# Performance work log

Hardware: AMD Instinct MI355X
Metric: run time of the kernel (lower is better)

Reference implementation:

```python
import jax, jax.numpy as jnp
import numpy as np

B, H, S, D = 4, 8, 8192, 64


def setup_inputs() -> dict:
    key = jax.random.key(0)
    kq, kk, kv_, kqm, kkm = jax.random.split(key, 5)
    q = jax.random.normal(kq, (B, H, S, D), dtype=jnp.float32)
    k = jax.random.normal(kk, (B, H, S, D), dtype=jnp.float32)
    v = jax.random.normal(kv_, (B, H, S, D), dtype=jnp.float32)
    q_mask = jax.random.randint(kqm, (B, S), 0, 2).astype(jnp.bool_)
    kv_mask = jax.random.randint(kkm, (B, S), 0, 2).astype(jnp.bool_)
    return {"q": q, "k": k, "v": v, "q_mask": q_mask, "kv_mask": kv_mask}


def reference(q, k, v, q_mask, kv_mask):
    # Linear (kernelized) attention branch: feature map phi(x) = elu(x) + 1
    qe = jax.nn.elu(q) + 1.0
    ke = jax.nn.elu(k) + 1.0
    qm = q_mask.astype(q.dtype)[:, None, :, None]   # [B,1,S,1]
    km = kv_mask.astype(q.dtype)[:, None, :, None]
    qe = qe * qm
    ke = ke * km
    ve = v * km
    s = v.shape[2]
    # kv: [B,H,D,D] contraction over kv sequence
    kv = jnp.einsum('bhsd,bhsc->bhdc', ke, ve / s)
    # normalizer per query position: [B,H,L]
    div = 1.0 / (jnp.einsum('bhld,bhsd->bhl', qe, ke) + 1e-6)
    out = s * jnp.einsum('bhld,bhdc,bhl->bhlc', qe, kv, div)
    return out
```

## Files before the change

### kernel.cpp

```cpp
#include <hip/hip_runtime.h>
#include <hip/hip_bf16.h>


#define S_LEN 8192
#define NBH 32
#define KVSTRIDE 4160

typedef __attribute__((ext_vector_type(8))) short short8;
typedef __attribute__((ext_vector_type(4))) float f32x4;

__device__ __forceinline__ float elu1(float x) {
  return x > 0.0f ? (x + 1.0f) : __expf(x);
}
__device__ __forceinline__ unsigned short f2bf(float x) {
  __hip_bfloat16 h = __float2bfloat16(x);
  union { __hip_bfloat16 b; unsigned short u; } cv; cv.b = h; return cv.u;
}
__device__ __forceinline__ float bf2f(unsigned short u) {
  return __uint_as_float(((unsigned)u) << 16);
}
__device__ __forceinline__ void split2(float x, unsigned short& hi, unsigned short& lo) {
  hi = f2bf(x);
  lo = f2bf(x - bf2f(hi));
}
__device__ __forceinline__ short8 ones8() {
  short8 o;
#pragma unroll
  for (int i = 0; i < 8; ++i) o[i] = (short)0x3F80;
  return o;
}

#define MFMA(a,b,c) __builtin_amdgcn_mfma_f32_16x16x32_bf16((a),(b),(c),0,0,0)

__global__ __launch_bounds__(256) void k1_partial(
    const float* __restrict__ kin, const float* __restrict__ vin,
    const int* __restrict__ kv_mask, float* __restrict__ partials, int seg_rows) {
  __shared__ unsigned short keT_h[64 * 72];
  __shared__ unsigned short keT_l[64 * 72];
  __shared__ unsigned short veT_h[64 * 72];
  __shared__ unsigned short veT_l[64 * 72];
  const int tid = threadIdx.x;
  const int seg = blockIdx.x, bh = blockIdx.y, b = bh >> 3;
  const int dp = tid & 31;
  const int so = tid >> 5;
  const int lane = tid & 63, w = tid >> 6;
  const int mrow = lane & 15, qd4 = lane >> 4;
  const short8 one = ones8();

  f32x4 acc[4]; f32x4 accs;
#pragma unroll
  for (int t = 0; t < 4; ++t) acc[t] = (f32x4){0.f, 0.f, 0.f, 0.f};
  accs = (f32x4){0.f, 0.f, 0.f, 0.f};

  const int rbase = seg * seg_rows;
  for (int t0 = 0; t0 < seg_rows; t0 += 64) {
    const int r0 = rbase + t0;
    const float* kp = kin + ((size_t)bh * S_LEN + r0 + so * 8) * 64 + dp * 2;
    const float* vp = vin + ((size_t)bh * S_LEN + r0 + so * 8) * 64 + dp * 2;
    union { unsigned short u[8]; uint4 v; } kh0, kh1, kl0, kl1, vh0, vh1, vl0, vl1;
#pragma unroll
    for (int r = 0; r < 8; ++r) {
      float m = kv_mask[b * S_LEN + r0 + so * 8 + r] ? 1.0f : 0.0f;
      float2 kw = *(const float2*)(kp + (size_t)r * 64);
      float2 vw = *(const float2*)(vp + (size_t)r * 64);
      float ka = elu1(kw.x) * m;
      float kb = elu1(kw.y) * m;
      float mv = m * (1.0f / 8192.0f);
      float va = vw.x * mv, vb = vw.y * mv;
      split2(ka, kh0.u[r], kl0.u[r]);
      split2(kb, kh1.u[r], kl1.u[r]);
      split2(va, vh0.u[r], vl0.u[r]);
      split2(vb, vh1.u[r], vl1.u[r]);
    }
    const int d0 = dp * 2;
    *(uint4*)&keT_h[(d0    ) * 72 + so * 8] = kh0.v;
    *(uint4*)&keT_h[(d0 + 1) * 72 + so * 8] = kh1.v;
    *(uint4*)&keT_l[(d0    ) * 72 + so * 8] = kl0.v;
    *(uint4*)&keT_l[(d0 + 1) * 72 + so * 8] = kl1.v;
    *(uint4*)&veT_h[(d0    ) * 72 + so * 8] = vh0.v;
    *(uint4*)&veT_h[(d0 + 1) * 72 + so * 8] = vh1.v;
    *(uint4*)&veT_l[(d0    ) * 72 + so * 8] = vl0.v;
    *(uint4*)&veT_l[(d0 + 1) * 72 + so * 8] = vl1.v;
    __syncthreads();
#pragma unroll
    for (int k0 = 0; k0 < 64; k0 += 32) {
      short8 a_h = *(const short8*)&keT_h[(w * 16 + mrow) * 72 + k0 + qd4 * 8];
      short8 a_l = *(const short8*)&keT_l[(w * 16 + mrow) * 72 + k0 + qd4 * 8];
      accs = MFMA(a_h, one, accs);
      accs = MFMA(a_l, one, accs);
#pragma unroll
      for (int t = 0; t < 4; ++t) {
        short8 b_h = *(const short8*)&veT_h[(t * 16 + mrow) * 72 + k0 + qd4 * 8];
        short8 b_l = *(const short8*)&veT_l[(t * 16 + mrow) * 72 + k0 + qd4 * 8];
        acc[t] = MFMA(a_h, b_h, acc[t]);
        acc[t] = MFMA(a_h, b_l, acc[t]);
        acc[t] = MFMA(a_l, b_h, acc[t]);
      }
    }
    __syncthreads();
  }
  float* p = partials + ((size_t)bh * gridDim.x + seg) * KVSTRIDE;
#pragma unroll
  for (int t = 0; t < 4; ++t)
#pragma unroll
    for (int r = 0; r < 4; ++r)
      p[(w * 16 + qd4 * 4 + r) * 64 + t * 16 + mrow] = acc[t][r];
  if (mrow == 0) {
#pragma unroll
    for (int r = 0; r < 4; ++r) p[4096 + w * 16 + qd4 * 4 + r] = accs[r];
  }
}

__global__ __launch_bounds__(256) void k2_reduce(
    const float* __restrict__ partials,
    unsigned short* __restrict__ kvTh, unsigned short* __restrict__ kvTl,
    unsigned short* __restrict__ ksh, unsigned short* __restrict__ ksl, int nchunk) {
  const int idx = blockIdx.x * 256 + threadIdx.x;
  if (idx >= NBH * KVSTRIDE) return;
  const int bh = idx / KVSTRIDE;
  const int e = idx - bh * KVSTRIDE;
  const float* p = partials + (size_t)bh * nchunk * KVSTRIDE + e;
  float s0 = 0.f, s1 = 0.f, s2 = 0.f, s3 = 0.f;
  int c = 0;
  for (; c + 4 <= nchunk; c += 4) {
    s0 += p[(size_t)(c + 0) * KVSTRIDE];
    s1 += p[(size_t)(c + 1) * KVSTRIDE];
    s2 += p[(size_t)(c + 2) * KVSTRIDE];
    s3 += p[(size_t)(c + 3) * KVSTRIDE];
  }
  for (; c < nchunk; ++c) s0 += p[(size_t)c * KVSTRIDE];
  float s = (s0 + s1) + (s2 + s3);
  unsigned short hi, lo;
  split2(s, hi, lo);
  if (e < 4096) {
    int d = e >> 6, cc = e & 63;
    kvTh[(size_t)bh * 4096 + cc * 64 + d] = hi;
    kvTl[(size_t)bh * 4096 + cc * 64 + d] = lo;
  } else {
    int d = e - 4096;
    ksh[bh * 64 + d] = hi;
    ksl[bh * 64 + d] = lo;
  }
}

__global__ __launch_bounds__(256) void k3_out(
    const float* __restrict__ qin, const int* __restrict__ q_mask,
    const unsigned short* __restrict__ kvTh_g, const unsigned short* __restrict__ kvTl_g,
    const unsigned short* __restrict__ ksh_g, const unsigned short* __restrict__ ksl_g,
    float* __restrict__ out) {
  __shared__ unsigned short qe_h[64 * 72];
  __shared__ unsigned short qe_l[64 * 72];
  __shared__ unsigned short kv_h[64 * 72];
  __shared__ unsigned short kv_l[64 * 72];
  __shared__ __align__(16) unsigned short ks_h[64];
  __shared__ __align__(16) unsigned short ks_l[64];
  const int tid = threadIdx.x;
  const int rb = blockIdx.x, bh = blockIdx.y, b = bh >> 3;
  const int r0 = rb * 64;
#pragma unroll
  for (int i = 0; i < 4; ++i) {
    int qd = i * 256 + tid;
    int l = qd >> 4, dq = qd & 15;
    float m = q_mask[b * S_LEN + r0 + l] ? 1.0f : 0.0f;
    float4 qw = *(const float4*)(qin + ((size_t)bh * S_LEN + r0 + l) * 64 + dq * 4);
    union { unsigned short u[4]; uint2 v; } h, lo;
    float e0 = elu1(qw.x) * m, e1 = elu1(qw.y) * m, e2 = elu1(qw.z) * m, e3 = elu1(qw.w) * m;
    split2(e0, h.u[0], lo.u[0]);
    split2(e1, h.u[1], lo.u[1]);
    split2(e2, h.u[2], lo.u[2]);
    split2(e3, h.u[3], lo.u[3]);
    *(uint2*)&qe_h[l * 72 + dq * 4] = h.v;
    *(uint2*)&qe_l[l * 72 + dq * 4] = lo.v;
  }
  for (int e = tid; e < 2048; e += 256) {
    int c = (e * 2) >> 6, d = (e * 2) & 63;
    *(unsigned*)&kv_h[c * 72 + d] = *(const unsigned*)(kvTh_g + (size_t)bh * 4096 + e * 2);
    *(unsigned*)&kv_l[c * 72 + d] = *(const unsigned*)(kvTl_g + (size_t)bh * 4096 + e * 2);
  }
  if (tid < 64) {
    ks_h[tid] = ksh_g[bh * 64 + tid];
    ks_l[tid] = ksl_g[bh * 64 + tid];
  }
  __syncthreads();
  const int lane = tid & 63, w = tid >> 6;
  const int mrow = lane & 15, qd4 = lane >> 4;
  f32x4 acc[4]; f32x4 accd;
#pragma unroll
  for (int t = 0; t < 4; ++t) acc[t] = (f32x4){0.f, 0.f, 0.f, 0.f};
  accd = (f32x4){0.f, 0.f, 0.f, 0.f};
#pragma unroll
  for (int k0 = 0; k0 < 64; k0 += 32) {
    short8 a_h = *(const short8*)&qe_h[(w * 16 + mrow) * 72 + k0 + qd4 * 8];
    short8 a_l = *(const short8*)&qe_l[(w * 16 + mrow) * 72 + k0 + qd4 * 8];
    short8 s_h = *(const short8*)&ks_h[k0 + qd4 * 8];
    short8 s_l = *(const short8*)&ks_l[k0 + qd4 * 8];
    accd = MFMA(a_h, s_h, accd);
    accd = MFMA(a_h, s_l, accd);
    accd = MFMA(a_l, s_h, accd);
#pragma unroll
    for (int t = 0; t < 4; ++t) {
      short8 b_h = *(const short8*)&kv_h[(t * 16 + mrow) * 72 + k0 + qd4 * 8];
      short8 b_l = *(const short8*)&kv_l[(t * 16 + mrow) * 72 + k0 + qd4 * 8];
      acc[t] = MFMA(a_h, b_h, acc[t]);
      acc[t] = MFMA(a_h, b_l, acc[t]);
      acc[t] = MFMA(a_l, b_h, acc[t]);
    }
  }
#pragma unroll
  for (int r = 0; r < 4; ++r) {
    float inv = 8192.0f / (accd[r] + 1e-6f);
    int row = r0 + w * 16 + qd4 * 4 + r;
#pragma unroll
    for (int t = 0; t < 4; ++t)
      out[((size_t)bh * S_LEN + row) * 64 + t * 16 + mrow] = acc[t][r] * inv;
  }
}

extern "C" void kernel_launch(void* const* d_in, const int* in_sizes, int n_in,
                              void* d_out, int out_size, void* d_ws, size_t ws_size,
                              hipStream_t stream) {
  const float* q = (const float*)d_in[0];
  const float* k = (const float*)d_in[1];
  const float* v = (const float*)d_in[2];
  const int* qm = (const int*)d_in[3];
  const int* km = (const int*)d_in[4];
  float* out = (float*)d_out;

  int nchunk = 32;
  while (nchunk > 1) {
    size_t need = (size_t)NBH * nchunk * KVSTRIDE * 4
                + (size_t)NBH * 4096 * 2 * 2 + (size_t)NBH * 64 * 2 * 2;
    if (need <= ws_size) break;
    nchunk >>= 1;
  }
  float* partials = (float*)d_ws;
  unsigned short* kvTh = (unsigned short*)(partials + (size_t)NBH * nchunk * KVSTRIDE);
  unsigned short* kvTl = kvTh + (size_t)NBH * 4096;
  unsigned short* ksh  = kvTl + (size_t)NBH * 4096;
  unsigned short* ksl  = ksh + NBH * 64;
  int seg_rows = S_LEN / nchunk;

  k1_partial<<<dim3(nchunk, NBH), 256, 0, stream>>>(k, v, km, partials, seg_rows);
  int n_elem = NBH * KVSTRIDE;
  k2_reduce<<<dim3((n_elem + 255) / 256), 256, 0, stream>>>(partials, kvTh, kvTl, ksh, ksl, nchunk);
  k3_out<<<dim3(S_LEN / 64, NBH), 256, 0, stream>>>(q, qm, kvTh, kvTl, ksh, ksl, out);
}
```

Before: 238.5 us.

## Drop LDS staging: build MFMA fragments directly from global loads in both kernels

k1 now gives each wave its own sequence segment and builds the bf16 hi/lo MFMA operands straight from global memory. This removes the shared-memory transpose and the block barriers. The K row-sum is done with scalar adds plus shuffles instead of MFMAs against a ones vector, and the chunk count doubles to 64 to keep parallelism up. k3 likewise loads Q and the KV tiles straight into registers with no LDS. The trade is strided, less coalesced global reads (column-wise per lane in k1), more register pressure from the 16 accumulators, and more partials for k2 to reduce.

```diff
diff --git a/kernel.cpp b/kernel.cpp
--- a/kernel.cpp
+++ b/kernel.cpp
@@ -13,8 +13,9 @@
   return x > 0.0f ? (x + 1.0f) : __expf(x);
 }
 __device__ __forceinline__ unsigned short f2bf(float x) {
-  __hip_bfloat16 h = __float2bfloat16(x);
-  union { __hip_bfloat16 b; unsigned short u; } cv; cv.b = h; return cv.u;
+  union { __hip_bfloat16 b; unsigned short u; } cv;
+  cv.b = __float2bfloat16(x);
+  return cv.u;
 }
 __device__ __forceinline__ float bf2f(unsigned short u) {
   return __uint_as_float(((unsigned)u) << 16);
@@ -23,91 +24,84 @@
   hi = f2bf(x);
   lo = f2bf(x - bf2f(hi));
 }
-__device__ __forceinline__ short8 ones8() {
-  short8 o;
-#pragma unroll
-  for (int i = 0; i < 8; ++i) o[i] = (short)0x3F80;
-  return o;
-}
 
 #define MFMA(a,b,c) __builtin_amdgcn_mfma_f32_16x16x32_bf16((a),(b),(c),0,0,0)
 
 __global__ __launch_bounds__(256) void k1_partial(
     const float* __restrict__ kin, const float* __restrict__ vin,
-    const int* __restrict__ kv_mask, float* __restrict__ partials, int seg_rows) {
-  __shared__ unsigned short keT_h[64 * 72];
-  __shared__ unsigned short keT_l[64 * 72];
-  __shared__ unsigned short veT_h[64 * 72];
-  __shared__ unsigned short veT_l[64 * 72];
+    const int* __restrict__ kv_mask, float* __restrict__ partials,
+    int nchunk, int seg_rows) {
   const int tid = threadIdx.x;
-  const int seg = blockIdx.x, bh = blockIdx.y, b = bh >> 3;
-  const int dp = tid & 31;
-  const int so = tid >> 5;
   const int lane = tid & 63, w = tid >> 6;
+  const int bh = blockIdx.y, b = bh >> 3;
+  const int seg = blockIdx.x * 4 + w;
   const int mrow = lane & 15, qd4 = lane >> 4;
-  const short8 one = ones8();
-
-  f32x4 acc[4]; f32x4 accs;
-#pragma unroll
-  for (int t = 0; t < 4; ++t) acc[t] = (f32x4){0.f, 0.f, 0.f, 0.f};
-  accs = (f32x4){0.f, 0.f, 0.f, 0.f};
-
-  const int rbase = seg * seg_rows;
-  for (int t0 = 0; t0 < seg_rows; t0 += 64) {
-    const int r0 = rbase + t0;
-    const float* kp = kin + ((size_t)bh * S_LEN + r0 + so * 8) * 64 + dp * 2;
-    const float* vp = vin + ((size_t)bh * S_LEN + r0 + so * 8) * 64 + dp * 2;
-    union { unsigned short u[8]; uint4 v; } kh0, kh1, kl0, kl1, vh0, vh1, vl0, vl1;
-#pragma unroll
-    for (int r = 0; r < 8; ++r) {
-      float m = kv_mask[b * S_LEN + r0 + so * 8 + r] ? 1.0f : 0.0f;
-      float2 kw = *(const float2*)(kp + (size_t)r * 64);
-      float2 vw = *(const float2*)(vp + (size_t)r * 64);
-      float ka = elu1(kw.x) * m;
-      float kb = elu1(kw.y) * m;
-      float mv = m * (1.0f / 8192.0f);
-      float va = vw.x * mv, vb = vw.y * mv;
-      split2(ka, kh0.u[r], kl0.u[r]);
-      split2(kb, kh1.u[r], kl1.u[r]);
-      split2(va, vh0.u[r], vl0.u[r]);
-      split2(vb, vh1.u[r], vl1.u[r]);
-    }
-    const int d0 = dp * 2;
-    *(uint4*)&keT_h[(d0    ) * 72 + so * 8] = kh0.v;
-    *(uint4*)&keT_h[(d0 + 1) * 72 + so * 8] = kh1.v;
-    *(uint4*)&keT_l[(d0    ) * 72 + so * 8] = kl0.v;
-    *(uint4*)&keT_l[(d0 + 1) * 72 + so * 8] = kl1.v;
-    *(uint4*)&veT_h[(d0    ) * 72 + so * 8] = vh0.v;
-    *(uint4*)&veT_h[(d0 + 1) * 72 + so * 8] = vh1.v;
-    *(uint4*)&veT_l[(d0    ) * 72 + so * 8] = vl0.v;
-    *(uint4*)&veT_l[(d0 + 1) * 72 + so * 8] = vl1.v;
-    __syncthreads();
-#pragma unroll
-    for (int k0 = 0; k0 < 64; k0 += 32) {
-      short8 a_h = *(const short8*)&keT_h[(w * 16 + mrow) * 72 + k0 + qd4 * 8];
-      short8 a_l = *(const short8*)&keT_l[(w * 16 + mrow) * 72 + k0 + qd4 * 8];
-      accs = MFMA(a_h, one, accs);
-      accs = MFMA(a_l, one, accs);
-#pragma unroll
-      for (int t = 0; t < 4; ++t) {
-        short8 b_h = *(const short8*)&veT_h[(t * 16 + mrow) * 72 + k0 + qd4 * 8];
-        short8 b_l = *(const short8*)&veT_l[(t * 16 + mrow) * 72 + k0 + qd4 * 8];
-        acc[t] = MFMA(a_h, b_h, acc[t]);
-        acc[t] = MFMA(a_h, b_l, acc[t]);
-        acc[t] = MFMA(a_l, b_h, acc[t]);
+
+  f32x4 acc[4][4];
+#pragma unroll
+  for (int i = 0; i < 4; ++i)
+#pragma unroll
+    for (int j = 0; j < 4; ++j) acc[i][j] = (f32x4){0.f, 0.f, 0.f, 0.f};
+  float ks[4] = {0.f, 0.f, 0.f, 0.f};
+
+  const float* kbase = kin + (size_t)bh * S_LEN * 64;
+  const float* vbase = vin + (size_t)bh * S_LEN * 64;
+  const int s_seg = seg * seg_rows;
+
+  for (int c0 = 0; c0 < seg_rows; c0 += 32) {
+    const int s0 = s_seg + c0 + qd4 * 8;
+    float mj[8];
+#pragma unroll
+    for (int j = 0; j < 8; ++j)
+      mj[j] = kv_mask[b * S_LEN + s0 + j] ? 1.0f : 0.0f;
+
+    short8 b_h[4], b_l[4];
+#pragma unroll
+    for (int td = 0; td < 4; ++td) {
+      const float* kp = kbase + (size_t)s0 * 64 + td * 16 + mrow;
+      union { unsigned short u[8]; short8 s8; } hh, ll;
+#pragma unroll
+      for (int j = 0; j < 8; ++j) {
+        float ke = elu1(kp[(size_t)j * 64]) * mj[j];
+        ks[td] += ke;
+        split2(ke, hh.u[j], ll.u[j]);
       }
-    }
-    __syncthreads();
-  }
-  float* p = partials + ((size_t)bh * gridDim.x + seg) * KVSTRIDE;
-#pragma unroll
-  for (int t = 0; t < 4; ++t)
-#pragma unroll
-    for (int r = 0; r < 4; ++r)
-      p[(w * 16 + qd4 * 4 + r) * 64 + t * 16 + mrow] = acc[t][r];
-  if (mrow == 0) {
-#pragma unroll
-    for (int r = 0; r < 4; ++r) p[4096 + w * 16 + qd4 * 4 + r] = accs[r];
+      b_h[td] = hh.s8; b_l[td] = ll.s8;
+    }
+#pragma unroll
+    for (int tc = 0; tc < 4; ++tc) {
+      const float* vp = vbase + (size_t)s0 * 64 + tc * 16 + mrow;
+      union { unsigned short u[8]; short8 s8; } hh, ll;
+#pragma unroll
+      for (int j = 0; j < 8; ++j) {
+        float ve = vp[(size_t)j * 64] * (mj[j] * (1.0f / 8192.0f));
+        split2(ve, hh.u[j], ll.u[j]);
+      }
+      short8 a_h = hh.s8, a_l = ll.s8;
+#pragma unroll
+      for (int td = 0; td < 4; ++td) {
+        acc[tc][td] = MFMA(a_h, b_h[td], acc[tc][td]);
+        acc[tc][td] = MFMA(a_h, b_l[td], acc[tc][td]);
+        acc[tc][td] = MFMA(a_l, b_h[td], acc[tc][td]);
+      }
+    }
+  }
+#pragma unroll
+  for (int td = 0; td < 4; ++td) {
+    ks[td] += __shfl_xor(ks[td], 32);
+    ks[td] += __shfl_xor(ks[td], 16);
+  }
+  float* p = partials + ((size_t)bh * nchunk + seg) * KVSTRIDE;
+#pragma unroll
+  for (int tc = 0; tc < 4; ++tc)
+#pragma unroll
+    for (int td = 0; td < 4; ++td)
+#pragma unroll
+      for (int r = 0; r < 4; ++r)
+        p[(tc * 16 + qd4 * 4 + r) * 64 + td * 16 + mrow] = acc[tc][td][r];
+  if (qd4 == 0) {
+#pragma unroll
+    for (int td = 0; td < 4; ++td) p[4096 + td * 16 + mrow] = ks[td];
   }
 }
 
@@ -133,86 +127,66 @@
   unsigned short hi, lo;
   split2(s, hi, lo);
   if (e < 4096) {
-    int d = e >> 6, cc = e & 63;
-    kvTh[(size_t)bh * 4096 + cc * 64 + d] = hi;
-    kvTl[(size_t)bh * 4096 + cc * 64 + d] = lo;
+    kvTh[(size_t)bh * 4096 + e] = hi;
+    kvTl[(size_t)bh * 4096 + e] = lo;
   } else {
-    int d = e - 4096;
-    ksh[bh * 64 + d] = hi;
-    ksl[bh * 64 + d] = lo;
+    ksh[bh * 64 + (e - 4096)] = hi;
+    ksl[bh * 64 + (e - 4096)] = lo;
   }
 }
 
 __global__ __launch_bounds__(256) void k3_out(
     const float* __restrict__ qin, const int* __restrict__ q_mask,
-    const unsigned short* __restrict__ kvTh_g, const unsigned short* __restrict__ kvTl_g,
-    const unsigned short* __restrict__ ksh_g, const unsigned short* __restrict__ ksl_g,
+    const unsigned short* __restrict__ kvTh, const unsigned short* __restrict__ kvTl,
+    const unsigned short* __restrict__ ksh, const unsigned short* __restrict__ ksl,
     float* __restrict__ out) {
-  __shared__ unsigned short qe_h[64 * 72];
-  __shared__ unsigned short qe_l[64 * 72];
-  __shared__ unsigned short kv_h[64 * 72];
-  __shared__ unsigned short kv_l[64 * 72];
-  __shared__ __align__(16) unsigned short ks_h[64];
-  __shared__ __align__(16) unsigned short ks_l[64];
-  const int tid = threadIdx.x;
+  const int tid = threadIdx.x, lane = tid & 63, w = tid >> 6;
   const int rb = blockIdx.x, bh = blockIdx.y, b = bh >> 3;
-  const int r0 = rb * 64;
-#pragma unroll
-  for (int i = 0; i < 4; ++i) {
-    int qd = i * 256 + tid;
-    int l = qd >> 4, dq = qd & 15;
-    float m = q_mask[b * S_LEN + r0 + l] ? 1.0f : 0.0f;
-    float4 qw = *(const float4*)(qin + ((size_t)bh * S_LEN + r0 + l) * 64 + dq * 4);
-    union { unsigned short u[4]; uint2 v; } h, lo;
-    float e0 = elu1(qw.x) * m, e1 = elu1(qw.y) * m, e2 = elu1(qw.z) * m, e3 = elu1(qw.w) * m;
-    split2(e0, h.u[0], lo.u[0]);
-    split2(e1, h.u[1], lo.u[1]);
-    split2(e2, h.u[2], lo.u[2]);
-    split2(e3, h.u[3], lo.u[3]);
-    *(uint2*)&qe_h[l * 72 + dq * 4] = h.v;
-    *(uint2*)&qe_l[l * 72 + dq * 4] = lo.v;
-  }
-  for (int e = tid; e < 2048; e += 256) {
-    int c = (e * 2) >> 6, d = (e * 2) & 63;
-    *(unsigned*)&kv_h[c * 72 + d] = *(const unsigned*)(kvTh_g + (size_t)bh * 4096 + e * 2);
-    *(unsigned*)&kv_l[c * 72 + d] = *(const unsigned*)(kvTl_g + (size_t)bh * 4096 + e * 2);
-  }
-  if (tid < 64) {
-    ks_h[tid] = ksh_g[bh * 64 + tid];
-    ks_l[tid] = ksl_g[bh * 64 + tid];
-  }
-  __syncthreads();
-  const int lane = tid & 63, w = tid >> 6;
   const int mrow = lane & 15, qd4 = lane >> 4;
-  f32x4 acc[4]; f32x4 accd;
+  const int l = rb * 64 + w * 16 + mrow;
+
+  const float m = q_mask[b * S_LEN + l] ? 1.0f : 0.0f;
+  f32x4 acc[4];
 #pragma unroll
   for (int t = 0; t < 4; ++t) acc[t] = (f32x4){0.f, 0.f, 0.f, 0.f};
-  accd = (f32x4){0.f, 0.f, 0.f, 0.f};
+  f32x4 accd = (f32x4){0.f, 0.f, 0.f, 0.f};
+
+  const unsigned short* kvh_b = kvTh + (size_t)bh * 4096;
+  const unsigned short* kvl_b = kvTl + (size_t)bh * 4096;
 #pragma unroll
   for (int k0 = 0; k0 < 64; k0 += 32) {
-    short8 a_h = *(const short8*)&qe_h[(w * 16 + mrow) * 72 + k0 + qd4 * 8];
-    short8 a_l = *(const short8*)&qe_l[(w * 16 + mrow) * 72 + k0 + qd4 * 8];
-    short8 s_h = *(const short8*)&ks_h[k0 + qd4 * 8];
-    short8 s_l = *(const short8*)&ks_l[k0 + qd4 * 8];
+    const float* qp = qin + ((size_t)bh * S_LEN + l) * 64 + k0 + qd4 * 8;
+    float4 q0 = *(const float4*)qp;
+    float4 q1 = *(const float4*)(qp + 4);
+    float xs[8] = {q0.x, q0.y, q0.z, q0.w, q1.x, q1.y, q1.z, q1.w};
+    union { unsigned short u[8]; short8 s8; } ah, al;
+#pragma unroll
+    for (int j = 0; j < 8; ++j) {
+      float qe = elu1(xs[j]) * m;
+      split2(qe, ah.u[j], al.u[j]);
+    }
+    short8 a_h = ah.s8, a_l = al.s8;
+    short8 s_h = *(const short8*)(ksh + bh * 64 + k0 + qd4 * 8);
+    short8 s_l = *(const short8*)(ksl + bh * 64 + k0 + qd4 * 8);
     accd = MFMA(a_h, s_h, accd);
     accd = MFMA(a_h, s_l, accd);
     accd = MFMA(a_l, s_h, accd);
 #pragma unroll
     for (int t = 0; t < 4; ++t) {
-      short8 b_h = *(const short8*)&kv_h[(t * 16 + mrow) * 72 + k0 + qd4 * 8];
-      short8 b_l = *(const short8*)&kv_l[(t * 16 + mrow) * 72 + k0 + qd4 * 8];
+      short8 b_h = *(const short8*)(kvh_b + (size_t)(t * 16 + mrow) * 64 + k0 + qd4 * 8);
+      short8 b_l = *(const short8*)(kvl_b + (size_t)(t * 16 + mrow) * 64 + k0 + qd4 * 8);
       acc[t] = MFMA(a_h, b_h, acc[t]);
       acc[t] = MFMA(a_h, b_l, acc[t]);
       acc[t] = MFMA(a_l, b_h, acc[t]);
     }
   }
+  const int row0 = rb * 64 + w * 16 + qd4 * 4;
 #pragma unroll
   for (int r = 0; r < 4; ++r) {
     float inv = 8192.0f / (accd[r] + 1e-6f);
-    int row = r0 + w * 16 + qd4 * 4 + r;
 #pragma unroll
     for (int t = 0; t < 4; ++t)
-      out[((size_t)bh * S_LEN + row) * 64 + t * 16 + mrow] = acc[t][r] * inv;
+      out[((size_t)bh * S_LEN + row0 + r) * 64 + t * 16 + mrow] = acc[t][r] * inv;
   }
 }
 
@@ -226,8 +200,8 @@
   const int* km = (const int*)d_in[4];
   float* out = (float*)d_out;
 
-  int nchunk = 32;
-  while (nchunk > 1) {
+  int nchunk = 64;
+  while (nchunk > 4) {
     size_t need = (size_t)NBH * nchunk * KVSTRIDE * 4
                 + (size_t)NBH * 4096 * 2 * 2 + (size_t)NBH * 64 * 2 * 2;
     if (need <= ws_size) break;
@@ -240,7 +214,7 @@
   unsigned short* ksl  = ksh + NBH * 64;
   int seg_rows = S_LEN / nchunk;
 
-  k1_partial<<<dim3(nchunk, NBH), 256, 0, stream>>>(k, v, km, partials, seg_rows);
+  k1_partial<<<dim3(nchunk / 4, NBH), 256, 0, stream>>>(k, v, km, partials, nchunk, seg_rows);
   int n_elem = NBH * KVSTRIDE;
   k2_reduce<<<dim3((n_elem + 255) / 256), 256, 0, stream>>>(partials, kvTh, kvTl, ksh, ksl, nchunk);
   k3_out<<<dim3(S_LEN / 64, NBH), 256, 0, stream>>>(q, qm, kvTh, kvTl, ksh, ksl, out);
```

Measured after the change: 265.5 us. +11.3%, slower.
